# Performance work log

Hardware: AMD Instinct MI355X
Metric: run time of the kernel (lower is better)

The kernel has to match this reference:

```python
import jax, jax.numpy as jnp
import numpy as np

N = 100_000   # nodes
IN = 256      # input feature size
H = 128       # hidden dim
OUT = 16      # output classes
R = 5         # relations
E = 100_000   # edges per relation
B = 2         # bases


def setup_inputs() -> dict:
    key = jax.random.key(0)
    ks = jax.random.split(key, 10)
    return {
        "x": jax.random.normal(ks[0], (N, IN), jnp.float32),
        "src": jax.random.randint(ks[1], (R, E), 0, N, dtype=jnp.int32),
        "dst": jax.random.randint(ks[2], (R, E), 0, N, dtype=jnp.int32),
        "w_embed": jax.random.normal(ks[3], (IN, H), jnp.float32) / np.sqrt(IN).astype(np.float32),
        "b_embed": jnp.zeros((H,), jnp.float32),
        "basis1": jax.random.normal(ks[4], (B, H, H), jnp.float32) / np.sqrt(H).astype(np.float32),
        "coef1": jax.random.normal(ks[5], (R, B), jnp.float32),
        "bias1": jnp.zeros((H,), jnp.float32),
        "basis2": jax.random.normal(ks[6], (B, H, OUT), jnp.float32) / np.sqrt(H).astype(np.float32),
        "coef2": jax.random.normal(ks[7], (R, B), jnp.float32),
        "bias2": jnp.zeros((OUT,), jnp.float32),
    }


def _rgcn_layer(h, src, dst, basis, coef, bias):
    # basis decomposition: W_r = sum_b coef[r,b] * V_b  -> [R, in, out]
    W = jnp.einsum('rb,bio->rio', coef, basis)

    def per_rel(s, d, w):
        msg = h[s] @ w                                        # [E, out] gather + GEMM
        agg = jax.ops.segment_sum(msg, d, num_segments=N)     # [N, out] scatter-add
        deg = jax.ops.segment_sum(jnp.ones((E,), h.dtype), d, num_segments=N)
        return agg / jnp.maximum(deg, 1.0)[:, None]           # fn.mean per relation

    out = jax.vmap(per_rel)(src, dst, W).sum(axis=0)          # 'sum' cross-relation reduce
    return out + bias


def reference(x, src, dst, w_embed, b_embed, basis1, coef1, bias1, basis2, coef2, bias2):
    h = x @ w_embed + b_embed                                 # EmbeddingLayer (Linear per ntype)
    h = jax.nn.relu(_rgcn_layer(h, src, dst, basis1, coef1, bias1))  # hidden RGCN layer, relu
    return _rgcn_layer(h, src, dst, basis2, coef2, bias2)     # output layer, no activation
```

## Files before the change

kernel.cpp:

```cpp
#include <hip/hip_runtime.h>
#include <hip/hip_bf16.h>
#include <cstddef>

namespace {

constexpr int N = 100000;
constexpr int IN = 256;
constexpr int H = 128;
constexpr int OUT = 16;
constexpr int R = 5;
constexpr int E = 100000;
constexpr int RE = R * E;
constexpr int NB = (N + 255) / 256;

using short8 = __attribute__((ext_vector_type(8))) short;
using f32x4 = __attribute__((ext_vector_type(4))) float;

__device__ __forceinline__ float b2f(unsigned int u16) {
  union { unsigned int i; float f; } v;
  v.i = u16 << 16;
  return v.f;
}
__device__ __forceinline__ unsigned short f2b(float f) {
  union { float f; unsigned int u; } v;
  v.f = f;
  unsigned int r = v.u + 0x7fffu + ((v.u >> 16) & 1u);
  return (unsigned short)(r >> 16);
}

__global__ void deg_count(const int* __restrict__ dst, float* __restrict__ deg,
                          int* __restrict__ degtot) {
  int i = blockIdx.x * 256 + threadIdx.x;
  if (i < RE) {
    int d = dst[i];
    atomicAdd(&deg[(i / E) * N + d], 1.0f);
    atomicAdd(&degtot[d], 1);
  }
}

__global__ void inv_deg_k(float* __restrict__ deg) {
  int i = blockIdx.x * 256 + threadIdx.x;
  if (i < R * N) deg[i] = 1.0f / fmaxf(deg[i], 1.0f);
}

__global__ void scan_blk(const int* __restrict__ in, int* __restrict__ part,
                         int* __restrict__ bsum, int n) {
  __shared__ int tmp[256];
  int tid = threadIdx.x;
  int gid = blockIdx.x * 256 + tid;
  int v = (gid < n) ? in[gid] : 0;
  tmp[tid] = v;
  __syncthreads();
  for (int o = 1; o < 256; o <<= 1) {
    int t = (tid >= o) ? tmp[tid - o] : 0;
    __syncthreads();
    tmp[tid] += t;
    __syncthreads();
  }
  if (gid < n) part[gid] = tmp[tid] - v;
  if (tid == 255) bsum[blockIdx.x] = tmp[255];
}

__global__ void scan_top(const int* __restrict__ bsum, int* __restrict__ bscan, int nb) {
  __shared__ int tmp[512];
  int tid = threadIdx.x;
  int v = (tid < nb) ? bsum[tid] : 0;
  tmp[tid] = v;
  __syncthreads();
  for (int o = 1; o < 512; o <<= 1) {
    int t = (tid >= o) ? tmp[tid - o] : 0;
    __syncthreads();
    tmp[tid] += t;
    __syncthreads();
  }
  if (tid < nb) bscan[tid] = tmp[tid] - v;
}

__global__ void scan_add(int* __restrict__ part, const int* __restrict__ bscan, int n) {
  int gid = blockIdx.x * 256 + threadIdx.x;
  if (gid < n) part[gid] += bscan[gid >> 8];
}

__global__ void fill_csr(const int* __restrict__ src, const int* __restrict__ dst,
                         const float* __restrict__ coef1, const float* __restrict__ coef2,
                         const float* __restrict__ invdeg, const int* __restrict__ off,
                         int* __restrict__ cursor, int* __restrict__ esrc,
                         float2* __restrict__ ecA, float2* __restrict__ ecB) {
  int i = blockIdx.x * 256 + threadIdx.x;
  if (i >= RE) return;
  int r = i / E;
  int d = dst[i];
  int slot = off[d] + atomicAdd(&cursor[d], 1);
  float id = invdeg[r * N + d];
  esrc[slot] = src[i];
  ecA[slot] = make_float2(coef1[2 * r] * id, coef1[2 * r + 1] * id);
  ecB[slot] = make_float2(coef2[2 * r] * id, coef2[2 * r + 1] * id);
}

__global__ void pack_w(const float* __restrict__ W, unsigned short* __restrict__ wp,
                       int NOUT, int total) {
  int i = blockIdx.x * 256 + threadIdx.x;
  if (i >= total) return;
  int ii = i & 7;
  int lane = (i >> 3) & 63;
  int fb = i >> 9;
  int NCT = NOUT >> 4;
  int kc = fb / NCT, ct = fb - kc * NCT;
  int k = kc * 32 + ((lane >> 4) << 3) + ii;
  int col = (ct << 4) + (lane & 15);
  wp[i] = f2b(W[(size_t)k * NOUT + col]);
}

__global__ void pack_b2(const float* __restrict__ basis2, unsigned short* __restrict__ wp) {
  int i = blockIdx.x * 256 + threadIdx.x;
  if (i >= 128 * 32) return;
  int ii = i & 7;
  int lane = (i >> 3) & 63;
  int fb = i >> 9;
  int kc = fb >> 1, ct = fb & 1;
  int k = kc * 32 + ((lane >> 4) << 3) + ii;
  wp[i] = f2b(basis2[((size_t)ct * 128 + k) * 16 + (lane & 15)]);
}

template <int K, int NOUT, bool AF32, bool BIAS, bool RELU>
__global__ __launch_bounds__(256) void gemm_mfma(
    const void* __restrict__ Araw, const unsigned short* __restrict__ wpack,
    const float* __restrict__ bias, unsigned short* __restrict__ C, int M) {
  constexpr int KC = K / 32;
  constexpr int NCT = NOUT / 16;
  __shared__ __align__(16) unsigned short alds[64][40];
  const int tid = threadIdx.x;
  const int wv = tid >> 6;
  const int lane = tid & 63;
  const int bm = blockIdx.x * 64;

  f32x4 acc[NCT];
#pragma unroll
  for (int t = 0; t < NCT; ++t) acc[t] = (f32x4){0.f, 0.f, 0.f, 0.f};

  const int srow = tid >> 2;
  const int skk = (tid & 3) * 8;
  int grow = bm + srow;
  if (grow > M - 1) grow = M - 1;

  const short8* wfrag = (const short8*)wpack;

  for (int kc = 0; kc < KC; ++kc) {
    if constexpr (AF32) {
      const float* ap = (const float*)Araw + (size_t)grow * K + kc * 32 + skk;
      float4 v0 = *(const float4*)ap;
      float4 v1 = *(const float4*)(ap + 4);
      short8 pk;
      pk[0] = (short)f2b(v0.x); pk[1] = (short)f2b(v0.y);
      pk[2] = (short)f2b(v0.z); pk[3] = (short)f2b(v0.w);
      pk[4] = (short)f2b(v1.x); pk[5] = (short)f2b(v1.y);
      pk[6] = (short)f2b(v1.z); pk[7] = (short)f2b(v1.w);
      *(short8*)&alds[srow][skk] = pk;
    } else {
      const unsigned short* ap = (const unsigned short*)Araw + (size_t)grow * K + kc * 32 + skk;
      *(short8*)&alds[srow][skk] = *(const short8*)ap;
    }
    __syncthreads();
    short8 af = *(const short8*)&alds[wv * 16 + (lane & 15)][(lane >> 4) * 8];
#pragma unroll
    for (int ct = 0; ct < NCT; ++ct) {
      short8 bf = wfrag[(kc * NCT + ct) * 64 + lane];
      acc[ct] = __builtin_amdgcn_mfma_f32_16x16x32_bf16(af, bf, acc[ct], 0, 0, 0);
    }
    __syncthreads();
  }

  const int c16 = lane & 15;
  const int rg = lane >> 4;
#pragma unroll
  for (int ct = 0; ct < NCT; ++ct) {
    int col = ct * 16 + c16;
    float bs = 0.f;
    if constexpr (BIAS) bs = bias[col];
#pragma unroll
    for (int i = 0; i < 4; ++i) {
      int row = bm + wv * 16 + rg * 4 + i;
      if (row < M) {
        float v = acc[ct][i] + bs;
        if constexpr (RELU) v = fmaxf(v, 0.f);
        C[(size_t)row * NOUT + col] = f2b(v);
      }
    }
  }
}

__global__ __launch_bounds__(256) void gather1(
    const int* __restrict__ off, const int* __restrict__ degtot,
    const int* __restrict__ esrc, const float2* __restrict__ ecA,
    const unsigned short* __restrict__ hbf, unsigned int* __restrict__ ubf) {
  int wid = blockIdx.x * 4 + (threadIdx.x >> 6);
  int lane = threadIdx.x & 63;
  if (wid >= N) return;
  int start = off[wid];
  int cnt = degtot[wid];
  float u0x = 0.f, u0y = 0.f, u1x = 0.f, u1y = 0.f;
  if (cnt > 0) {
    int s = esrc[start];
    float2 c = ecA[start];
    unsigned int hv = ((const unsigned int*)(hbf + (size_t)s * 128))[lane];
    for (int j = 1; j < cnt; ++j) {
      int sn = esrc[start + j];
      float2 cn = ecA[start + j];
      unsigned int hvn = ((const unsigned int*)(hbf + (size_t)sn * 128))[lane];
      float hx = b2f(hv & 0xffffu), hy = b2f(hv >> 16);
      u0x = fmaf(c.x, hx, u0x); u0y = fmaf(c.x, hy, u0y);
      u1x = fmaf(c.y, hx, u1x); u1y = fmaf(c.y, hy, u1y);
      s = sn; c = cn; hv = hvn;
    }
    float hx = b2f(hv & 0xffffu), hy = b2f(hv >> 16);
    u0x = fmaf(c.x, hx, u0x); u0y = fmaf(c.x, hy, u0y);
    u1x = fmaf(c.y, hx, u1x); u1y = fmaf(c.y, hy, u1y);
  }
  unsigned int* ur = ubf + (size_t)wid * 128;
  ur[lane]      = (unsigned int)f2b(u0x) | ((unsigned int)f2b(u0y) << 16);
  ur[64 + lane] = (unsigned int)f2b(u1x) | ((unsigned int)f2b(u1y) << 16);
}

__global__ __launch_bounds__(256) void gather2(
    const int* __restrict__ off, const int* __restrict__ degtot,
    const int* __restrict__ esrc, const float2* __restrict__ ecB,
    const unsigned short* __restrict__ qbf, const float* __restrict__ bias2,
    float* __restrict__ out) {
  int node = blockIdx.x * 16 + (threadIdx.x >> 4);
  int k = threadIdx.x & 15;
  if (node >= N) return;
  int start = off[node];
  int cnt = degtot[node];
  float acc = bias2[k];
  for (int j = 0; j < cnt; ++j) {
    int s = esrc[start + j];
    float2 c = ecB[start + j];
    acc = fmaf(c.x, b2f(qbf[(size_t)s * 32 + k]), acc);
    acc = fmaf(c.y, b2f(qbf[(size_t)s * 32 + 16 + k]), acc);
  }
  out[(size_t)node * 16 + k] = acc;
}

}

extern "C" void kernel_launch(void* const* d_in, const int* in_sizes, int n_in,
                              void* d_out, int out_size, void* d_ws, size_t ws_size,
                              hipStream_t stream) {
  const float* x       = (const float*)d_in[0];
  const int*   src     = (const int*)d_in[1];
  const int*   dst     = (const int*)d_in[2];
  const float* w_embed = (const float*)d_in[3];
  const float* b_embed = (const float*)d_in[4];
  const float* basis1  = (const float*)d_in[5];
  const float* coef1   = (const float*)d_in[6];
  const float* bias1   = (const float*)d_in[7];
  const float* basis2  = (const float*)d_in[8];
  const float* coef2   = (const float*)d_in[9];
  const float* bias2   = (const float*)d_in[10];
  float* out = (float*)d_out;

  float2* ecA = (float2*)d_ws;
  float2* ecB = ecA + RE;
  float*  invdeg = (float*)(ecB + RE);
  int*    degtot = (int*)(invdeg + (size_t)R * N);
  int*    off    = degtot + N;
  int*    bsum   = off + N;
  int*    bscan  = bsum + 512;
  int*    cursor = bscan + 512;
  int*    esrc   = cursor + N;
  unsigned short* wp1  = (unsigned short*)(esrc + RE);
  unsigned short* wpB1 = wp1 + 256 * 128;
  unsigned short* wpB2 = wpB1 + 256 * 128;
  unsigned short* h_bf = wpB2 + 128 * 32;
  unsigned short* u_bf = h_bf + (size_t)N * 128;
  unsigned short* h2_bf = h_bf;
  unsigned short* q_bf  = u_bf;

  dim3 b256(256);
  hipMemsetAsync(invdeg, 0, (size_t)R * N * sizeof(float), stream);
  hipMemsetAsync(degtot, 0, (size_t)N * sizeof(int), stream);
  hipMemsetAsync(cursor, 0, (size_t)N * sizeof(int), stream);

  deg_count<<<(RE + 255) / 256, b256, 0, stream>>>(dst, invdeg, degtot);
  inv_deg_k<<<(R * N + 255) / 256, b256, 0, stream>>>(invdeg);
  scan_blk<<<NB, b256, 0, stream>>>(degtot, off, bsum, N);
  scan_top<<<1, dim3(512), 0, stream>>>(bsum, bscan, NB);
  scan_add<<<NB, b256, 0, stream>>>(off, bscan, N);
  fill_csr<<<(RE + 255) / 256, b256, 0, stream>>>(src, dst, coef1, coef2, invdeg,
                                                  off, cursor, esrc, ecA, ecB);
  pack_w<<<(256 * 128 + 255) / 256, b256, 0, stream>>>(w_embed, wp1, 128, 256 * 128);
  pack_w<<<(256 * 128 + 255) / 256, b256, 0, stream>>>(basis1, wpB1, 128, 256 * 128);
  pack_b2<<<(128 * 32 + 255) / 256, b256, 0, stream>>>(basis2, wpB2);

  int gblocks = (N + 63) / 64;
  gemm_mfma<256, 128, true, true, false>
      <<<gblocks, b256, 0, stream>>>(x, wp1, b_embed, h_bf, N);
  gather1<<<(N + 3) / 4, b256, 0, stream>>>(off, degtot, esrc, ecA, h_bf,
                                            (unsigned int*)u_bf);
  gemm_mfma<256, 128, false, true, true>
      <<<gblocks, b256, 0, stream>>>(u_bf, wpB1, bias1, h2_bf, N);
  gemm_mfma<128, 32, false, false, false>
      <<<gblocks, b256, 0, stream>>>(h2_bf, wpB2, nullptr, q_bf, N);
  gather2<<<(N + 15) / 16, b256, 0, stream>>>(off, degtot, esrc, ecB, q_bf, bias2, out);
}
```

Measured before the change: 420.1 us.

## Fuse layer-1 and layer-2 GEMMs and drop LDS staging in MFMA GEMMs

Replaces the generic LDS-staged GEMM with per-wave 32-row tiles that load A fragments straight from global memory into registers, removing the block-wide syncthreads per K step. The hidden-layer GEMM (with bias and ReLU) is fused with the output-basis GEMM. The ReLU output goes through a per-wave LDS tile instead of a round trip of h2 through global memory, which saves one kernel launch and an N x 128 bf16 write and read. In exchange, register pressure rises (16 accumulators per lane), the kernels skip row bounds checks because N is a multiple of 32, and the q buffer is moved to a separate workspace region.

```diff
diff --git a/kernel.cpp b/kernel.cpp
--- a/kernel.cpp
+++ b/kernel.cpp
@@ -122,71 +122,139 @@
   wp[i] = f2b(basis2[((size_t)ct * 128 + k) * 16 + (lane & 15)]);
 }
 
-template <int K, int NOUT, bool AF32, bool BIAS, bool RELU>
-__global__ __launch_bounds__(256) void gemm_mfma(
-    const void* __restrict__ Araw, const unsigned short* __restrict__ wpack,
-    const float* __restrict__ bias, unsigned short* __restrict__ C, int M) {
-  constexpr int KC = K / 32;
-  constexpr int NCT = NOUT / 16;
-  __shared__ __align__(16) unsigned short alds[64][40];
+__global__ __launch_bounds__(256) void gemm_embed(
+    const float* __restrict__ x, const unsigned short* __restrict__ wpack,
+    const float* __restrict__ bias, unsigned short* __restrict__ C) {
   const int tid = threadIdx.x;
+  const int lane = tid & 63;
+  const int wave = (blockIdx.x * 256 + tid) >> 6;
+  const int base = wave * 32;
+  if (base >= N) return;
+  const int r = lane & 15, g = lane >> 4;
+  const short8* wfrag = (const short8*)wpack;
+
+  f32x4 acc[2][8];
+#pragma unroll
+  for (int t = 0; t < 2; ++t)
+#pragma unroll
+    for (int ct = 0; ct < 8; ++ct) acc[t][ct] = (f32x4){0.f, 0.f, 0.f, 0.f};
+
+  const float* a0 = x + (size_t)(base + r) * IN + g * 8;
+  const float* a1 = a0 + (size_t)16 * IN;
+
+#pragma unroll
+  for (int kc = 0; kc < 8; ++kc) {
+    float4 v0 = *(const float4*)(a0 + kc * 32);
+    float4 v1 = *(const float4*)(a0 + kc * 32 + 4);
+    float4 v2 = *(const float4*)(a1 + kc * 32);
+    float4 v3 = *(const float4*)(a1 + kc * 32 + 4);
+    short8 af0, af1;
+    af0[0] = (short)f2b(v0.x); af0[1] = (short)f2b(v0.y);
+    af0[2] = (short)f2b(v0.z); af0[3] = (short)f2b(v0.w);
+    af0[4] = (short)f2b(v1.x); af0[5] = (short)f2b(v1.y);
+    af0[6] = (short)f2b(v1.z); af0[7] = (short)f2b(v1.w);
+    af1[0] = (short)f2b(v2.x); af1[1] = (short)f2b(v2.y);
+    af1[2] = (short)f2b(v2.z); af1[3] = (short)f2b(v2.w);
+    af1[4] = (short)f2b(v3.x); af1[5] = (short)f2b(v3.y);
+    af1[6] = (short)f2b(v3.z); af1[7] = (short)f2b(v3.w);
+#pragma unroll
+    for (int ct = 0; ct < 8; ++ct) {
+      short8 bf = wfrag[(kc * 8 + ct) * 64 + lane];
+      acc[0][ct] = __builtin_amdgcn_mfma_f32_16x16x32_bf16(af0, bf, acc[0][ct], 0, 0, 0);
+      acc[1][ct] = __builtin_amdgcn_mfma_f32_16x16x32_bf16(af1, bf, acc[1][ct], 0, 0, 0);
+    }
+  }
+
+#pragma unroll
+  for (int t = 0; t < 2; ++t)
+#pragma unroll
+    for (int ct = 0; ct < 8; ++ct) {
+      int col = ct * 16 + r;
+      float bs = bias[col];
+#pragma unroll
+      for (int i = 0; i < 4; ++i)
+        C[(size_t)(base + t * 16 + g * 4 + i) * H + col] = f2b(acc[t][ct][i] + bs);
+    }
+}
+
+__global__ __launch_bounds__(256) void gemm_fused(
+    const unsigned short* __restrict__ u, const unsigned short* __restrict__ wp1,
+    const float* __restrict__ bias1, const unsigned short* __restrict__ wp2,
+    unsigned short* __restrict__ q) {
+  constexpr int LP2 = 132;
+  __shared__ unsigned short hl[4][32][LP2];
+  const int tid = threadIdx.x;
+  const int lane = tid & 63;
   const int wv = tid >> 6;
-  const int lane = tid & 63;
-  const int bm = blockIdx.x * 64;
-
-  f32x4 acc[NCT];
-#pragma unroll
-  for (int t = 0; t < NCT; ++t) acc[t] = (f32x4){0.f, 0.f, 0.f, 0.f};
-
-  const int srow = tid >> 2;
-  const int skk = (tid & 3) * 8;
-  int grow = bm + srow;
-  if (grow > M - 1) grow = M - 1;
-
-  const short8* wfrag = (const short8*)wpack;
-
-  for (int kc = 0; kc < KC; ++kc) {
-    if constexpr (AF32) {
-      const float* ap = (const float*)Araw + (size_t)grow * K + kc * 32 + skk;
-      float4 v0 = *(const float4*)ap;
-      float4 v1 = *(const float4*)(ap + 4);
-      short8 pk;
-      pk[0] = (short)f2b(v0.x); pk[1] = (short)f2b(v0.y);
-      pk[2] = (short)f2b(v0.z); pk[3] = (short)f2b(v0.w);
-      pk[4] = (short)f2b(v1.x); pk[5] = (short)f2b(v1.y);
-      pk[6] = (short)f2b(v1.z); pk[7] = (short)f2b(v1.w);
-      *(short8*)&alds[srow][skk] = pk;
-    } else {
-      const unsigned short* ap = (const unsigned short*)Araw + (size_t)grow * K + kc * 32 + skk;
-      *(short8*)&alds[srow][skk] = *(const short8*)ap;
-    }
-    __syncthreads();
-    short8 af = *(const short8*)&alds[wv * 16 + (lane & 15)][(lane >> 4) * 8];
-#pragma unroll
-    for (int ct = 0; ct < NCT; ++ct) {
-      short8 bf = wfrag[(kc * NCT + ct) * 64 + lane];
-      acc[ct] = __builtin_amdgcn_mfma_f32_16x16x32_bf16(af, bf, acc[ct], 0, 0, 0);
-    }
-    __syncthreads();
-  }
-
-  const int c16 = lane & 15;
-  const int rg = lane >> 4;
-#pragma unroll
-  for (int ct = 0; ct < NCT; ++ct) {
-    int col = ct * 16 + c16;
-    float bs = 0.f;
-    if constexpr (BIAS) bs = bias[col];
-#pragma unroll
-    for (int i = 0; i < 4; ++i) {
-      int row = bm + wv * 16 + rg * 4 + i;
-      if (row < M) {
-        float v = acc[ct][i] + bs;
-        if constexpr (RELU) v = fmaxf(v, 0.f);
-        C[(size_t)row * NOUT + col] = f2b(v);
-      }
-    }
-  }
+  const int wave = (blockIdx.x * 256 + tid) >> 6;
+  const int base = wave * 32;
+  if (base >= N) return;
+  const int r = lane & 15, g = lane >> 4;
+  const short8* wf1 = (const short8*)wp1;
+  const short8* wf2 = (const short8*)wp2;
+
+  f32x4 acc[2][8];
+#pragma unroll
+  for (int t = 0; t < 2; ++t)
+#pragma unroll
+    for (int ct = 0; ct < 8; ++ct) acc[t][ct] = (f32x4){0.f, 0.f, 0.f, 0.f};
+
+  const unsigned short* a0 = u + (size_t)(base + r) * 256 + g * 8;
+  const unsigned short* a1 = a0 + (size_t)16 * 256;
+
+#pragma unroll
+  for (int kc = 0; kc < 8; ++kc) {
+    short8 af0 = *(const short8*)(a0 + kc * 32);
+    short8 af1 = *(const short8*)(a1 + kc * 32);
+#pragma unroll
+    for (int ct = 0; ct < 8; ++ct) {
+      short8 bf = wf1[(kc * 8 + ct) * 64 + lane];
+      acc[0][ct] = __builtin_amdgcn_mfma_f32_16x16x32_bf16(af0, bf, acc[0][ct], 0, 0, 0);
+      acc[1][ct] = __builtin_amdgcn_mfma_f32_16x16x32_bf16(af1, bf, acc[1][ct], 0, 0, 0);
+    }
+  }
+
+#pragma unroll
+  for (int t = 0; t < 2; ++t)
+#pragma unroll
+    for (int ct = 0; ct < 8; ++ct) {
+      int col = ct * 16 + r;
+      float bs = bias1[col];
+#pragma unroll
+      for (int i = 0; i < 4; ++i)
+        hl[wv][t * 16 + g * 4 + i][col] = f2b(fmaxf(acc[t][ct][i] + bs, 0.f));
+    }
+
+  asm volatile("s_waitcnt lgkmcnt(0)" ::: "memory");
+  __builtin_amdgcn_sched_barrier(0);
+
+  f32x4 acc2[2][2];
+#pragma unroll
+  for (int t = 0; t < 2; ++t)
+#pragma unroll
+    for (int ct = 0; ct < 2; ++ct) acc2[t][ct] = (f32x4){0.f, 0.f, 0.f, 0.f};
+
+#pragma unroll
+  for (int kc = 0; kc < 4; ++kc) {
+    short8 af0 = *(const short8*)&hl[wv][r][kc * 32 + g * 8];
+    short8 af1 = *(const short8*)&hl[wv][16 + r][kc * 32 + g * 8];
+#pragma unroll
+    for (int ct = 0; ct < 2; ++ct) {
+      short8 bf = wf2[(kc * 2 + ct) * 64 + lane];
+      acc2[0][ct] = __builtin_amdgcn_mfma_f32_16x16x32_bf16(af0, bf, acc2[0][ct], 0, 0, 0);
+      acc2[1][ct] = __builtin_amdgcn_mfma_f32_16x16x32_bf16(af1, bf, acc2[1][ct], 0, 0, 0);
+    }
+  }
+
+#pragma unroll
+  for (int t = 0; t < 2; ++t)
+#pragma unroll
+    for (int ct = 0; ct < 2; ++ct) {
+      int col = ct * 16 + r;
+#pragma unroll
+      for (int i = 0; i < 4; ++i)
+        q[(size_t)(base + t * 16 + g * 4 + i) * 32 + col] = f2b(acc2[t][ct][i]);
+    }
 }
 
 __global__ __launch_bounds__(256) void gather1(
@@ -273,8 +341,7 @@
   unsigned short* wpB2 = wpB1 + 256 * 128;
   unsigned short* h_bf = wpB2 + 128 * 32;
   unsigned short* u_bf = h_bf + (size_t)N * 128;
-  unsigned short* h2_bf = h_bf;
-  unsigned short* q_bf  = u_bf;
+  unsigned short* q_bf = u_bf + (size_t)N * 256;
 
   dim3 b256(256);
   hipMemsetAsync(invdeg, 0, (size_t)R * N * sizeof(float), stream);
@@ -292,14 +359,11 @@
   pack_w<<<(256 * 128 + 255) / 256, b256, 0, stream>>>(basis1, wpB1, 128, 256 * 128);
   pack_b2<<<(128 * 32 + 255) / 256, b256, 0, stream>>>(basis2, wpB2);
 
-  int gblocks = (N + 63) / 64;
-  gemm_mfma<256, 128, true, true, false>
-      <<<gblocks, b256, 0, stream>>>(x, wp1, b_embed, h_bf, N);
+  int gwaves = (N + 31) / 32;
+  int gblocks = (gwaves + 3) / 4;
+  gemm_embed<<<gblocks, b256, 0, stream>>>(x, wp1, b_embed, h_bf);
   gather1<<<(N + 3) / 4, b256, 0, stream>>>(off, degtot, esrc, ecA, h_bf,
                                             (unsigned int*)u_bf);
-  gemm_mfma<256, 128, false, true, true>
-      <<<gblocks, b256, 0, stream>>>(u_bf, wpB1, bias1, h2_bf, N);
-  gemm_mfma<128, 32, false, false, false>
-      <<<gblocks, b256, 0, stream>>>(h2_bf, wpB2, nullptr, q_bf, N);
+  gemm_fused<<<gblocks, b256, 0, stream>>>(u_bf, wpB1, bias1, wpB2, q_bf);
   gather2<<<(N + 15) / 16, b256, 0, stream>>>(off, degtot, esrc, ecB, q_bf, bias2, out);
 }
```

Measured after the change: 427.8 us. Within noise of the previous version (+1.8%).
